# Performance work log

Measured on AMD Instinct MI355X. Metric: run time of the kernel, lower is better.

The kernel has to match this reference:

```python
import jax, jax.numpy as jnp
import numpy as np

N_EMBD = 768
N_HEAD = 12
B, T = 2, 2048
EPS = 1e-5


def _layernorm(x, g, b):
    mu = jnp.mean(x, axis=-1, keepdims=True)
    var = jnp.var(x, axis=-1, keepdims=True)
    return (x - mu) * jax.lax.rsqrt(var + EPS) * g + b


def _mha(q, k, v, causal):
    # q,k,v: [B,T,C] already projected
    Bq, Tq, C = q.shape
    d = C // N_HEAD
    q = q.reshape(Bq, Tq, N_HEAD, d).transpose(0, 2, 1, 3)  # b h t d
    k = k.reshape(Bq, Tq, N_HEAD, d).transpose(0, 2, 1, 3)
    v = v.reshape(Bq, Tq, N_HEAD, d).transpose(0, 2, 1, 3)
    scores = jnp.einsum('bhqd,bhkd->bhqk', q, k) * (1.0 / jnp.sqrt(jnp.float32(d)))
    if causal:
        mask = jnp.tril(jnp.ones((Tq, Tq), dtype=bool))
        scores = jnp.where(mask[None, None], scores, jnp.float32(-jnp.inf))
    att = jax.nn.softmax(scores, axis=-1)
    y = jnp.einsum('bhqk,bhkd->bhqd', att, v)
    return y.transpose(0, 2, 1, 3).reshape(Bq, Tq, C)


def setup_inputs() -> dict:
    key = jax.random.key(0)
    ks = iter(jax.random.split(key, 32))
    C = N_EMBD

    def lin(kk, din, dout):
        w = jax.random.normal(kk, (din, dout), jnp.float32) * (1.0 / np.sqrt(din))
        return w

    inp = {
        'x': jax.random.normal(next(ks), (B, T, C), jnp.float32),
        'encoder_output': jax.random.normal(next(ks), (B, T, C), jnp.float32),
        'ln1_g': jnp.ones((C,), jnp.float32), 'ln1_b': jnp.zeros((C,), jnp.float32),
        'attn_qkv_w': lin(next(ks), C, 3 * C), 'attn_qkv_b': jnp.zeros((3 * C,), jnp.float32),
        'attn_proj_w': lin(next(ks), C, C), 'attn_proj_b': jnp.zeros((C,), jnp.float32),
        'ln2_g': jnp.ones((C,), jnp.float32), 'ln2_b': jnp.zeros((C,), jnp.float32),
        'ca_q_w': lin(next(ks), C, C), 'ca_q_b': jnp.zeros((C,), jnp.float32),
        'ca_k_w': lin(next(ks), C, C), 'ca_k_b': jnp.zeros((C,), jnp.float32),
        'ca_v_w': lin(next(ks), C, C), 'ca_v_b': jnp.zeros((C,), jnp.float32),
        'ca_o_w': lin(next(ks), C, C), 'ca_o_b': jnp.zeros((C,), jnp.float32),
        'ln3_g': jnp.ones((C,), jnp.float32), 'ln3_b': jnp.zeros((C,), jnp.float32),
        'fc_w': lin(next(ks), C, 4 * C), 'fc_b': jnp.zeros((4 * C,), jnp.float32),
        'fc2_w': lin(next(ks), 4 * C, C), 'fc2_b': jnp.zeros((C,), jnp.float32),
    }
    return inp


def reference(x, encoder_output, ln1_g, ln1_b, attn_qkv_w, attn_qkv_b,
              attn_proj_w, attn_proj_b, ln2_g, ln2_b,
              ca_q_w, ca_q_b, ca_k_w, ca_k_b, ca_v_w, ca_v_b, ca_o_w, ca_o_b,
              ln3_g, ln3_b, fc_w, fc_b, fc2_w, fc2_b):
    C = N_EMBD
    # causal self-attention
    qkv = x @ attn_qkv_w + attn_qkv_b
    q, k, v = qkv[..., :C], qkv[..., C:2 * C], qkv[..., 2 * C:]
    sa = _mha(q, k, v, causal=True) @ attn_proj_w + attn_proj_b
    x = _layernorm(sa + x, ln1_g, ln1_b)
    # cross-attention
    cq = x @ ca_q_w + ca_q_b
    ck = encoder_output @ ca_k_w + ca_k_b
    cv = encoder_output @ ca_v_w + ca_v_b
    ca = _mha(cq, ck, cv, causal=False) @ ca_o_w + ca_o_b
    x = _layernorm(ca + x, ln2_g, ln2_b)
    # MLP
    h = jax.nn.relu(x @ fc_w + fc_b) @ fc2_w + fc2_b
    x = _layernorm(h + x, ln3_g, ln3_b)
    return x
```

## Files before the change

kernel.cpp:

```cpp
#include <hip/hip_runtime.h>


#define C_EMBD 768
#define NHEAD  12
#define HD     64
#define TB     2048
#define BB     2
#define MTOK   (BB*TB)

typedef __bf16 bf16_8 __attribute__((ext_vector_type(8)));
typedef float  f32x4  __attribute__((ext_vector_type(4)));

#define EXP2(x) exp2f(x)

__device__ __forceinline__ unsigned short f2bf(float f) {
    union { __bf16 h; unsigned short u; } c;
    c.h = (__bf16)f;
    return c.u;
}

#define GLOAD_LDS16(gsrc, ldst) \
    __builtin_amdgcn_global_load_lds( \
        (const __attribute__((address_space(1))) void*)(gsrc), \
        (__attribute__((address_space(3))) void*)(ldst), 16, 0, 0)

__global__ __launch_bounds__(256) void k_conv_bf16(const float* __restrict__ in,
                                                   unsigned short* __restrict__ out) {
    int i = blockIdx.x * 256 + threadIdx.x;
    float4 v = ((const float4*)in)[i];
    ushort4 o;
    o.x = f2bf(v.x); o.y = f2bf(v.y); o.z = f2bf(v.z); o.w = f2bf(v.w);
    ((ushort4*)out)[i] = o;
}

__global__ __launch_bounds__(256) void k_concat_bias(const float* __restrict__ a,
                                                     const float* __restrict__ b,
                                                     float* __restrict__ dst) {
    int i = blockIdx.x * 256 + threadIdx.x;
    if (i < C_EMBD) { dst[i] = a[i]; dst[C_EMBD + i] = b[i]; }
}

__global__ __launch_bounds__(256) void k_scale_bias(const float* __restrict__ b,
                                                    float* __restrict__ dst,
                                                    int n, float s, int lim) {
    int i = blockIdx.x * 256 + threadIdx.x;
    if (i < n) dst[i] = b[i] * (i < lim ? s : 1.0f);
}

__global__ __launch_bounds__(256) void k_transpose_w(const float* __restrict__ W,
                                                     unsigned short* __restrict__ Wt,
                                                     int K, int N,
                                                     float scale, int scaleLim) {
    __shared__ float tile[32][33];
    int tx = threadIdx.x, ty = threadIdx.y;
    int n0 = blockIdx.x * 32, k0 = blockIdx.y * 32;
#pragma unroll
    for (int i = 0; i < 4; ++i)
        tile[ty + 8*i][tx] = W[(size_t)(k0 + ty + 8*i) * N + n0 + tx];
    __syncthreads();
#pragma unroll
    for (int i = 0; i < 4; ++i) {
        int nrow = n0 + ty + 8*i;
        float s = (nrow < scaleLim) ? scale : 1.0f;
        Wt[(size_t)nrow * K + k0 + tx] = f2bf(tile[tx][ty + 8*i] * s);
    }
}

template<int BM, bool OUT_BF16, bool ADD_RES, bool RELU>
__global__ __launch_bounds__(256) void k_gemm_bt(
        const unsigned short* __restrict__ A,
        const unsigned short* __restrict__ Bt,
        const float* __restrict__ bias,
        const float* __restrict__ res,
        void* __restrict__ Cout,
        int M, int N, int K) {
    constexpr int MF = BM / 32;
    __shared__ unsigned short As[BM * 32];
    __shared__ unsigned short Bs[128 * 32];
    int tid  = threadIdx.x;
    int lane = tid & 63, wave = tid >> 6;
    int l16 = lane & 15, lg = lane >> 4;
    int wm = (wave >> 1) * (BM / 2), wn = (wave & 1) * 64;
    int bm = blockIdx.x * BM, bn = blockIdx.y * 128;

    f32x4 acc[MF][4] = {};

    for (int k0 = 0; k0 < K; k0 += 32) {
        __syncthreads();
#pragma unroll
        for (int i = 0; i < BM / 64; ++i) {
            int chunk = i * 256 + tid;
            GLOAD_LDS16(A + (size_t)(bm + (chunk >> 2)) * K + k0 + (chunk & 3) * 8,
                        As + (size_t)(i * 256 + wave * 64) * 8);
        }
#pragma unroll
        for (int i = 0; i < 2; ++i) {
            int chunk = i * 256 + tid;
            GLOAD_LDS16(Bt + (size_t)(bn + (chunk >> 2)) * K + k0 + (chunk & 3) * 8,
                        Bs + (size_t)(i * 256 + wave * 64) * 8);
        }
        __syncthreads();
        bf16_8 af[MF], bfr[4];
#pragma unroll
        for (int m = 0; m < MF; ++m)
            af[m]  = *(const bf16_8*)(As + (size_t)(wm + m*16 + l16) * 32 + lg * 8);
#pragma unroll
        for (int n = 0; n < 4; ++n)
            bfr[n] = *(const bf16_8*)(Bs + (size_t)(wn + n*16 + l16) * 32 + lg * 8);
#pragma unroll
        for (int m = 0; m < MF; ++m)
#pragma unroll
            for (int n = 0; n < 4; ++n)
                acc[m][n] = __builtin_amdgcn_mfma_f32_16x16x32_bf16(af[m], bfr[n], acc[m][n], 0, 0, 0);
    }

#pragma unroll
    for (int m = 0; m < MF; ++m) {
#pragma unroll
        for (int n = 0; n < 4; ++n) {
            int col = bn + wn + n*16 + l16;
            float bv = bias[col];
#pragma unroll
            for (int r = 0; r < 4; ++r) {
                int row = bm + wm + m*16 + lg*4 + r;
                float v = acc[m][n][r] + bv;
                if (ADD_RES) v += res[(size_t)row * N + col];
                if (RELU)    v = fmaxf(v, 0.f);
                if (OUT_BF16) ((unsigned short*)Cout)[(size_t)row * N + col] = f2bf(v);
                else          ((float*)Cout)[(size_t)row * N + col] = v;
            }
        }
    }
}

template<bool CAUSAL>
__global__ __launch_bounds__(256) void k_attn(
        const unsigned short* __restrict__ Qp,
        const unsigned short* __restrict__ Kp,
        const unsigned short* __restrict__ Vp,
        unsigned short* __restrict__ Yp,
        int strideQ, int strideKV) {
    __shared__ __bf16 Ks[64][72];
    __shared__ __bf16 Vt[64][72];
    __shared__ __bf16 Ps[4][16][72];
    int tid  = threadIdx.x;
    int lane = tid & 63, wave = tid >> 6;
    int l16 = lane & 15, lg = lane >> 4;
    int bh = blockIdx.y;
    int b = bh / NHEAD, h = bh - b * NHEAD;
    int qt = CAUSAL ? (gridDim.x - 1 - blockIdx.x) : blockIdx.x;
    int wq = qt * 64 + wave * 16;

    const unsigned short* Qb = Qp + (size_t)b * TB * strideQ  + h * HD;
    const unsigned short* Kb = Kp + (size_t)b * TB * strideKV + h * HD;
    const unsigned short* Vb = Vp + (size_t)b * TB * strideKV + h * HD;

    bf16_8 qf0 = *(const bf16_8*)(Qb + (size_t)(wq + l16) * strideQ + lg * 8);
    bf16_8 qf1 = *(const bf16_8*)(Qb + (size_t)(wq + l16) * strideQ + 32 + lg * 8);

    bf16_8 vones;
#pragma unroll
    for (int j = 0; j < 8; ++j) vones[j] = (__bf16)1.0f;

    int kr = tid >> 3, kc = (tid & 7) * 8;
    int vk2 = (tid & 31) * 2;
    int vd0 = (tid >> 5) * 8;

    const unsigned short* gK0 = Kb + (size_t)kr  * strideKV + kc;
    const unsigned short* gK1 = gK0 + (size_t)32 * strideKV;
    const unsigned short* gV0 = Vb + (size_t)vk2 * strideKV + vd0;
    const unsigned short* gV1 = gV0 + strideKV;
    const size_t stepKV = (size_t)64 * strideKV;

    int4 kA = *(const int4*)gK0;
    int4 kB = *(const int4*)gK1;
    unsigned vp[8];
    {
        int4 va = *(const int4*)gV0, vb2 = *(const int4*)gV1;
        const unsigned short* pa = (const unsigned short*)&va;
        const unsigned short* pb = (const unsigned short*)&vb2;
#pragma unroll
        for (int j = 0; j < 8; ++j) vp[j] = (unsigned)pa[j] | ((unsigned)pb[j] << 16);
    }

    f32x4 o[4] = {};
    float m_run[4], l_run[4];
#pragma unroll
    for (int r = 0; r < 4; ++r) { m_run[r] = -1e30f; l_run[r] = 0.f; }

    int ktEnd = CAUSAL ? (qt + 1) : (TB / 64);
    for (int kt = 0; kt < ktEnd; ++kt) {
        __syncthreads();
        *(int4*)(&Ks[kr][kc])      = kA;
        *(int4*)(&Ks[kr + 32][kc]) = kB;
#pragma unroll
        for (int j = 0; j < 8; ++j)
            *(unsigned*)(&Vt[vd0 + j][vk2]) = vp[j];
        __syncthreads();

        if (kt + 1 < ktEnd) {
            gK0 += stepKV; gK1 += stepKV; gV0 += stepKV; gV1 += stepKV;
            kA = *(const int4*)gK0;
            kB = *(const int4*)gK1;
            int4 va = *(const int4*)gV0, vb2 = *(const int4*)gV1;
            const unsigned short* pa = (const unsigned short*)&va;
            const unsigned short* pb = (const unsigned short*)&vb2;
#pragma unroll
            for (int j = 0; j < 8; ++j) vp[j] = (unsigned)pa[j] | ((unsigned)pb[j] << 16);
        }

        f32x4 s[4];
#pragma unroll
        for (int n = 0; n < 4; ++n) {
            f32x4 z = {};
            bf16_8 kf0 = *(const bf16_8*)(&Ks[n*16 + l16][lg*8]);
            bf16_8 kf1 = *(const bf16_8*)(&Ks[n*16 + l16][32 + lg*8]);
            z = __builtin_amdgcn_mfma_f32_16x16x32_bf16(qf0, kf0, z, 0, 0, 0);
            z = __builtin_amdgcn_mfma_f32_16x16x32_bf16(qf1, kf1, z, 0, 0, 0);
            s[n] = z;
        }
        if (CAUSAL && kt == qt) {
#pragma unroll
            for (int n = 0; n < 4; ++n)
#pragma unroll
                for (int r = 0; r < 4; ++r)
                    if (kt*64 + n*16 + l16 > wq + lg*4 + r) s[n][r] = -1e30f;
        }
        float mx[4];
#pragma unroll
        for (int r = 0; r < 4; ++r)
            mx[r] = fmaxf(fmaxf(s[0][r], s[1][r]), fmaxf(s[2][r], s[3][r]));
#pragma unroll
        for (int off = 1; off < 16; off <<= 1)
#pragma unroll
            for (int r = 0; r < 4; ++r)
                mx[r] = fmaxf(mx[r], __shfl_xor(mx[r], off, 64));
        bool big = (mx[0] > m_run[0] + 8.f) | (mx[1] > m_run[1] + 8.f) |
                   (mx[2] > m_run[2] + 8.f) | (mx[3] > m_run[3] + 8.f);
        if (__any(big)) {
#pragma unroll
            for (int r = 0; r < 4; ++r) {
                float mnew = fmaxf(m_run[r], mx[r]);
                float sf = EXP2(m_run[r] - mnew);
                m_run[r] = mnew;
                l_run[r] *= sf;
#pragma unroll
                for (int n = 0; n < 4; ++n) o[n][r] *= sf;
            }
        }
#pragma unroll
        for (int n = 0; n < 4; ++n)
#pragma unroll
            for (int r = 0; r < 4; ++r)
                Ps[wave][lg*4 + r][n*16 + l16] = (__bf16)EXP2(s[n][r] - m_run[r]);

        f32x4 zsum = {};
#pragma unroll
        for (int kk = 0; kk < 2; ++kk) {
            bf16_8 pa = *(const bf16_8*)(&Ps[wave][l16][kk*32 + lg*8]);
            zsum = __builtin_amdgcn_mfma_f32_16x16x32_bf16(pa, vones, zsum, 0, 0, 0);
#pragma unroll
            for (int n = 0; n < 4; ++n) {
                bf16_8 vf = *(const bf16_8*)(&Vt[n*16 + l16][kk*32 + lg*8]);
                o[n] = __builtin_amdgcn_mfma_f32_16x16x32_bf16(pa, vf, o[n], 0, 0, 0);
            }
        }
#pragma unroll
        for (int r = 0; r < 4; ++r) l_run[r] += zsum[r];
    }

#pragma unroll
    for (int r = 0; r < 4; ++r) {
        float rl = 1.0f / l_run[r];
        int token = b * TB + wq + lg*4 + r;
#pragma unroll
        for (int n = 0; n < 4; ++n)
            Yp[(size_t)token * C_EMBD + h * HD + n*16 + l16] = f2bf(o[n][r] * rl);
    }
}

template<bool WF32, bool WBF16>
__global__ __launch_bounds__(256) void k_ln(const float* __restrict__ in,
                                            const float* __restrict__ g,
                                            const float* __restrict__ bb,
                                            float* __restrict__ outf,
                                            unsigned short* __restrict__ outb) {
    int row = blockIdx.x;
    const float* x = in + (size_t)row * C_EMBD;
    float v[3], s1 = 0.f, s2 = 0.f;
#pragma unroll
    for (int i = 0; i < 3; ++i) {
        v[i] = x[threadIdx.x + i * 256];
        s1 += v[i];
        s2 += v[i] * v[i];
    }
#pragma unroll
    for (int off = 1; off < 64; off <<= 1) {
        s1 += __shfl_xor(s1, off, 64);
        s2 += __shfl_xor(s2, off, 64);
    }
    __shared__ float red[8];
    int wave = threadIdx.x >> 6, lane = threadIdx.x & 63;
    if (lane == 0) { red[wave] = s1; red[4 + wave] = s2; }
    __syncthreads();
    s1 = red[0] + red[1] + red[2] + red[3];
    s2 = red[4] + red[5] + red[6] + red[7];
    float mu  = s1 * (1.f / C_EMBD);
    float var = s2 * (1.f / C_EMBD) - mu * mu;
    float rs  = rsqrtf(var + 1e-5f);
#pragma unroll
    for (int i = 0; i < 3; ++i) {
        int c = threadIdx.x + i * 256;
        float y = (v[i] - mu) * rs * g[c] + bb[c];
        if (WF32)  outf[(size_t)row * C_EMBD + c] = y;
        if (WBF16) outb[(size_t)row * C_EMBD + c] = f2bf(y);
    }
}

extern "C" void kernel_launch(void* const* d_in, const int* in_sizes, int n_in,
                              void* d_out, int out_size, void* d_ws, size_t ws_size,
                              hipStream_t stream) {
    (void)in_sizes; (void)n_in; (void)out_size; (void)ws_size;
    const float* x      = (const float*)d_in[0];
    const float* enc    = (const float*)d_in[1];
    const float* ln1_g  = (const float*)d_in[2];
    const float* ln1_b  = (const float*)d_in[3];
    const float* qkv_w  = (const float*)d_in[4];
    const float* qkv_b  = (const float*)d_in[5];
    const float* proj_w = (const float*)d_in[6];
    const float* proj_b = (const float*)d_in[7];
    const float* ln2_g  = (const float*)d_in[8];
    const float* ln2_b  = (const float*)d_in[9];
    const float* caq_w  = (const float*)d_in[10];
    const float* caq_b  = (const float*)d_in[11];
    const float* cak_w  = (const float*)d_in[12];
    const float* cak_b  = (const float*)d_in[13];
    const float* cav_w  = (const float*)d_in[14];
    const float* cav_b  = (const float*)d_in[15];
    const float* cao_w  = (const float*)d_in[16];
    const float* cao_b  = (const float*)d_in[17];
    const float* ln3_g  = (const float*)d_in[18];
    const float* ln3_b  = (const float*)d_in[19];
    const float* fc_w   = (const float*)d_in[20];
    const float* fc_b   = (const float*)d_in[21];
    const float* fc2_w  = (const float*)d_in[22];
    const float* fc2_b  = (const float*)d_in[23];
    float* out = (float*)d_out;

    char* ws = (char*)d_ws;
    auto us = [&](size_t off) { return (unsigned short*)(ws + off); };
    auto fl = [&](size_t off) { return (float*)(ws + off); };

    const size_t O_WQKV  = 0;
    const size_t O_WPROJ = 3538944;
    const size_t O_WCQ   = 4718592;
    const size_t O_WCK   = 5898240;
    const size_t O_WCV   = 7077888;
    const size_t O_WCO   = 8257536;
    const size_t O_WFC   = 9437184;
    const size_t O_WFC2  = 14155776;
    const size_t O_XBF   = 18874368;
    const size_t O_ENCBF = 25165824;
    const size_t O_QKVBF = 31457280;
    const size_t O_Q2    = O_QKVBF;
    const size_t O_KV2   = O_QKVBF + 6291456;
    const size_t O_YBF   = 50331648;
    const size_t O_RESF  = 56623104;
    const size_t O_X1F   = 69206016;
    const size_t O_X1BF  = 81788928;
    const size_t O_X2F   = 88080384;
    const size_t O_X2BF  = 100663296;
    const size_t O_HBF   = 106954752;
    const size_t O_BKV   = O_HBF;
    const size_t O_BQKV  = O_HBF + 8192;
    const size_t O_BCQ   = O_HBF + 20480;

    const float SC2 = 0.125f * 1.44269504f;
    dim3 tb(32, 8);

    k_conv_bf16<<<3072, 256, 0, stream>>>(x,   us(O_XBF));
    k_conv_bf16<<<3072, 256, 0, stream>>>(enc, us(O_ENCBF));
    k_concat_bias<<<3, 256, 0, stream>>>(cak_b, cav_b, fl(O_BKV));
    k_scale_bias<<<9, 256, 0, stream>>>(qkv_b, fl(O_BQKV), 2304, SC2, 768);
    k_scale_bias<<<3, 256, 0, stream>>>(caq_b, fl(O_BCQ),   768, SC2, 768);

    k_transpose_w<<<dim3(2304/32,  768/32), tb, 0, stream>>>(qkv_w,  us(O_WQKV),  768, 2304, SC2, 768);
    k_transpose_w<<<dim3( 768/32,  768/32), tb, 0, stream>>>(proj_w, us(O_WPROJ), 768,  768, 1.f, 0);
    k_transpose_w<<<dim3( 768/32,  768/32), tb, 0, stream>>>(caq_w,  us(O_WCQ),   768,  768, SC2, 768);
    k_transpose_w<<<dim3( 768/32,  768/32), tb, 0, stream>>>(cak_w,  us(O_WCK),   768,  768, 1.f, 0);
    k_transpose_w<<<dim3( 768/32,  768/32), tb, 0, stream>>>(cav_w,  us(O_WCV),   768,  768, 1.f, 0);
    k_transpose_w<<<dim3( 768/32,  768/32), tb, 0, stream>>>(cao_w,  us(O_WCO),   768,  768, 1.f, 0);
    k_transpose_w<<<dim3(3072/32,  768/32), tb, 0, stream>>>(fc_w,   us(O_WFC),   768, 3072, 1.f, 0);
    k_transpose_w<<<dim3( 768/32, 3072/32), tb, 0, stream>>>(fc2_w,  us(O_WFC2), 3072,  768, 1.f, 0);

    k_gemm_bt<128, true,  false, false><<<dim3(32, 18), 256, 0, stream>>>(
        us(O_XBF), us(O_WQKV), fl(O_BQKV), nullptr, us(O_QKVBF), MTOK, 2304, 768);
    k_attn<true><<<dim3(TB/64, BB*NHEAD), 256, 0, stream>>>(
        us(O_QKVBF), us(O_QKVBF) + 768, us(O_QKVBF) + 1536, us(O_YBF), 2304, 2304);
    k_gemm_bt<64, false, true,  false><<<dim3(64, 6), 256, 0, stream>>>(
        us(O_YBF), us(O_WPROJ), proj_b, x, fl(O_RESF), MTOK, 768, 768);
    k_ln<true, true><<<MTOK, 256, 0, stream>>>(fl(O_RESF), ln1_g, ln1_b, fl(O_X1F), us(O_X1BF));
    k_gemm_bt<64, true,  false, false><<<dim3(64, 6), 256, 0, stream>>>(
        us(O_X1BF),  us(O_WCQ), fl(O_BCQ), nullptr, us(O_Q2), MTOK, 768, 768);
    k_gemm_bt<128, true,  false, false><<<dim3(32, 12), 256, 0, stream>>>(
        us(O_ENCBF), us(O_WCK), fl(O_BKV), nullptr, us(O_KV2), MTOK, 1536, 768);
    k_attn<false><<<dim3(TB/64, BB*NHEAD), 256, 0, stream>>>(
        us(O_Q2), us(O_KV2), us(O_KV2) + 768, us(O_YBF), 768, 1536);
    k_gemm_bt<64, false, true,  false><<<dim3(64, 6), 256, 0, stream>>>(
        us(O_YBF), us(O_WCO), cao_b, fl(O_X1F), fl(O_RESF), MTOK, 768, 768);
    k_ln<true, true><<<MTOK, 256, 0, stream>>>(fl(O_RESF), ln2_g, ln2_b, fl(O_X2F), us(O_X2BF));
    k_gemm_bt<128, true,  false, true ><<<dim3(32, 24), 256, 0, stream>>>(
        us(O_X2BF), us(O_WFC), fc_b, nullptr, us(O_HBF), MTOK, 3072, 768);
    k_gemm_bt<64, false, true,  false><<<dim3(64, 6), 256, 0, stream>>>(
        us(O_HBF), us(O_WFC2), fc2_b, fl(O_X2F), fl(O_RESF), MTOK, 768, 3072);
    k_ln<true, false><<<MTOK, 256, 0, stream>>>(fl(O_RESF), ln3_g, ln3_b, out, nullptr);
}
```

Baseline: 531.2 us.

## Fuse preprocessing launches and pair causal attention tiles per block

All weight transposes, input bf16 conversions and bias preparation are merged into one kernel that picks its job from the block index, replacing thirteen small launches with one. The causal attention grid is halved, and each block now handles query tile i and its mirror tile 31-i in sequence, so every block does about the same number of KV iterations. This is meant to cut launch overhead and the tail imbalance of triangular work. In exchange there are fewer blocks (384) to spread across the CUs, and the two passes run serially inside each block.

```diff
diff --git a/kernel.cpp b/kernel.cpp
--- a/kernel.cpp
+++ b/kernel.cpp
@@ -24,45 +24,67 @@
         (const __attribute__((address_space(1))) void*)(gsrc), \
         (__attribute__((address_space(3))) void*)(ldst), 16, 0, 0)
 
-__global__ __launch_bounds__(256) void k_conv_bf16(const float* __restrict__ in,
-                                                   unsigned short* __restrict__ out) {
-    int i = blockIdx.x * 256 + threadIdx.x;
-    float4 v = ((const float4*)in)[i];
-    ushort4 o;
-    o.x = f2bf(v.x); o.y = f2bf(v.y); o.z = f2bf(v.z); o.w = f2bf(v.w);
-    ((ushort4*)out)[i] = o;
-}
-
-__global__ __launch_bounds__(256) void k_concat_bias(const float* __restrict__ a,
-                                                     const float* __restrict__ b,
-                                                     float* __restrict__ dst) {
-    int i = blockIdx.x * 256 + threadIdx.x;
-    if (i < C_EMBD) { dst[i] = a[i]; dst[C_EMBD + i] = b[i]; }
-}
-
-__global__ __launch_bounds__(256) void k_scale_bias(const float* __restrict__ b,
-                                                    float* __restrict__ dst,
-                                                    int n, float s, int lim) {
-    int i = blockIdx.x * 256 + threadIdx.x;
-    if (i < n) dst[i] = b[i] * (i < lim ? s : 1.0f);
-}
-
-__global__ __launch_bounds__(256) void k_transpose_w(const float* __restrict__ W,
-                                                     unsigned short* __restrict__ Wt,
-                                                     int K, int N,
-                                                     float scale, int scaleLim) {
+__global__ __launch_bounds__(256) void k_preproc(
+        const float* __restrict__ x,     const float* __restrict__ enc,
+        const float* __restrict__ qkv_w, const float* __restrict__ proj_w,
+        const float* __restrict__ caq_w, const float* __restrict__ cak_w,
+        const float* __restrict__ cav_w, const float* __restrict__ cao_w,
+        const float* __restrict__ fc_w,  const float* __restrict__ fc2_w,
+        const float* __restrict__ qkv_b, const float* __restrict__ caq_b,
+        const float* __restrict__ cak_b, const float* __restrict__ cav_b,
+        unsigned short* __restrict__ xbf,  unsigned short* __restrict__ encbf,
+        unsigned short* __restrict__ wqkv, unsigned short* __restrict__ wproj,
+        unsigned short* __restrict__ wcq,  unsigned short* __restrict__ wck,
+        unsigned short* __restrict__ wcv,  unsigned short* __restrict__ wco,
+        unsigned short* __restrict__ wfc,  unsigned short* __restrict__ wfc2,
+        float* __restrict__ bqkv, float* __restrict__ bkv, float* __restrict__ bcq,
+        float sc2) {
     __shared__ float tile[32][33];
-    int tx = threadIdx.x, ty = threadIdx.y;
-    int n0 = blockIdx.x * 32, k0 = blockIdx.y * 32;
-#pragma unroll
-    for (int i = 0; i < 4; ++i)
-        tile[ty + 8*i][tx] = W[(size_t)(k0 + ty + 8*i) * N + n0 + tx];
-    __syncthreads();
-#pragma unroll
-    for (int i = 0; i < 4; ++i) {
-        int nrow = n0 + ty + 8*i;
-        float s = (nrow < scaleLim) ? scale : 1.0f;
-        Wt[(size_t)nrow * K + k0 + tx] = f2bf(tile[tx][ty + 8*i] * s);
+    int b = blockIdx.x, tid = threadIdx.x;
+    if (b < 9216) {
+        const float* W; unsigned short* Wt; int K, N, t; float sc; int slim;
+        if      (b < 1728) { W=qkv_w;  Wt=wqkv;  K=768;  N=2304; t=b;      sc=sc2; slim=768; }
+        else if (b < 2304) { W=proj_w; Wt=wproj; K=768;  N=768;  t=b-1728; sc=1.f; slim=0;   }
+        else if (b < 2880) { W=caq_w;  Wt=wcq;   K=768;  N=768;  t=b-2304; sc=sc2; slim=768; }
+        else if (b < 3456) { W=cak_w;  Wt=wck;   K=768;  N=768;  t=b-2880; sc=1.f; slim=0;   }
+        else if (b < 4032) { W=cav_w;  Wt=wcv;   K=768;  N=768;  t=b-3456; sc=1.f; slim=0;   }
+        else if (b < 4608) { W=cao_w;  Wt=wco;   K=768;  N=768;  t=b-4032; sc=1.f; slim=0;   }
+        else if (b < 6912) { W=fc_w;   Wt=wfc;   K=768;  N=3072; t=b-4608; sc=1.f; slim=0;   }
+        else               { W=fc2_w;  Wt=wfc2;  K=3072; N=768;  t=b-6912; sc=1.f; slim=0;   }
+        int ntx = N >> 5;
+        int n0 = (t % ntx) * 32, k0 = (t / ntx) * 32;
+        int tx = tid & 31, ty = tid >> 5;
+#pragma unroll
+        for (int i = 0; i < 4; ++i)
+            tile[ty + 8*i][tx] = W[(size_t)(k0 + ty + 8*i) * N + n0 + tx];
+        __syncthreads();
+#pragma unroll
+        for (int i = 0; i < 4; ++i) {
+            int nrow = n0 + ty + 8*i;
+            float s = (nrow < slim) ? sc : 1.0f;
+            Wt[(size_t)nrow * K + k0 + tx] = f2bf(tile[tx][ty + 8*i] * s);
+        }
+    } else if (b < 15360) {
+        int b2 = b - 9216;
+        const float* src = (b2 < 3072) ? x   : enc;
+        unsigned short* dst = (b2 < 3072) ? xbf : encbf;
+        int i = (b2 < 3072 ? b2 : b2 - 3072) * 256 + tid;
+        float4 v = ((const float4*)src)[i];
+        ushort4 o;
+        o.x = f2bf(v.x); o.y = f2bf(v.y); o.z = f2bf(v.z); o.w = f2bf(v.w);
+        ((ushort4*)dst)[i] = o;
+    } else {
+        int b3 = b - 15360;
+        if (b3 < 9) {
+            int i = b3 * 256 + tid;
+            if (i < 2304) bqkv[i] = qkv_b[i] * (i < 768 ? sc2 : 1.0f);
+        } else if (b3 < 12) {
+            int i = (b3 - 9) * 256 + tid;
+            if (i < 768) { bkv[i] = cak_b[i]; bkv[768 + i] = cav_b[i]; }
+        } else {
+            int i = (b3 - 12) * 256 + tid;
+            if (i < 768) bcq[i] = caq_b[i] * sc2;
+        }
     }
 }
 
@@ -148,16 +170,11 @@
     int l16 = lane & 15, lg = lane >> 4;
     int bh = blockIdx.y;
     int b = bh / NHEAD, h = bh - b * NHEAD;
-    int qt = CAUSAL ? (gridDim.x - 1 - blockIdx.x) : blockIdx.x;
-    int wq = qt * 64 + wave * 16;
 
     const unsigned short* Qb = Qp + (size_t)b * TB * strideQ  + h * HD;
     const unsigned short* Kb = Kp + (size_t)b * TB * strideKV + h * HD;
     const unsigned short* Vb = Vp + (size_t)b * TB * strideKV + h * HD;
 
-    bf16_8 qf0 = *(const bf16_8*)(Qb + (size_t)(wq + l16) * strideQ + lg * 8);
-    bf16_8 qf1 = *(const bf16_8*)(Qb + (size_t)(wq + l16) * strideQ + 32 + lg * 8);
-
     bf16_8 vones;
 #pragma unroll
     for (int j = 0; j < 8; ++j) vones[j] = (__bf16)1.0f;
@@ -165,43 +182,26 @@
     int kr = tid >> 3, kc = (tid & 7) * 8;
     int vk2 = (tid & 31) * 2;
     int vd0 = (tid >> 5) * 8;
-
-    const unsigned short* gK0 = Kb + (size_t)kr  * strideKV + kc;
-    const unsigned short* gK1 = gK0 + (size_t)32 * strideKV;
-    const unsigned short* gV0 = Vb + (size_t)vk2 * strideKV + vd0;
-    const unsigned short* gV1 = gV0 + strideKV;
     const size_t stepKV = (size_t)64 * strideKV;
 
-    int4 kA = *(const int4*)gK0;
-    int4 kB = *(const int4*)gK1;
-    unsigned vp[8];
-    {
-        int4 va = *(const int4*)gV0, vb2 = *(const int4*)gV1;
-        const unsigned short* pa = (const unsigned short*)&va;
-        const unsigned short* pb = (const unsigned short*)&vb2;
-#pragma unroll
-        for (int j = 0; j < 8; ++j) vp[j] = (unsigned)pa[j] | ((unsigned)pb[j] << 16);
-    }
-
-    f32x4 o[4] = {};
-    float m_run[4], l_run[4];
-#pragma unroll
-    for (int r = 0; r < 4; ++r) { m_run[r] = -1e30f; l_run[r] = 0.f; }
-
-    int ktEnd = CAUSAL ? (qt + 1) : (TB / 64);
-    for (int kt = 0; kt < ktEnd; ++kt) {
-        __syncthreads();
-        *(int4*)(&Ks[kr][kc])      = kA;
-        *(int4*)(&Ks[kr + 32][kc]) = kB;
-#pragma unroll
-        for (int j = 0; j < 8; ++j)
-            *(unsigned*)(&Vt[vd0 + j][vk2]) = vp[j];
-        __syncthreads();
-
-        if (kt + 1 < ktEnd) {
-            gK0 += stepKV; gK1 += stepKV; gV0 += stepKV; gV1 += stepKV;
-            kA = *(const int4*)gK0;
-            kB = *(const int4*)gK1;
+    const int npass = CAUSAL ? 2 : 1;
+    for (int pass = 0; pass < npass; ++pass) {
+        int qt = CAUSAL ? (pass == 0 ? (TB/64 - 1 - (int)blockIdx.x) : (int)blockIdx.x)
+                        : (int)blockIdx.x;
+        int wq = qt * 64 + wave * 16;
+
+        bf16_8 qf0 = *(const bf16_8*)(Qb + (size_t)(wq + l16) * strideQ + lg * 8);
+        bf16_8 qf1 = *(const bf16_8*)(Qb + (size_t)(wq + l16) * strideQ + 32 + lg * 8);
+
+        const unsigned short* gK0 = Kb + (size_t)kr  * strideKV + kc;
+        const unsigned short* gK1 = gK0 + (size_t)32 * strideKV;
+        const unsigned short* gV0 = Vb + (size_t)vk2 * strideKV + vd0;
+        const unsigned short* gV1 = gV0 + strideKV;
+
+        int4 kA = *(const int4*)gK0;
+        int4 kB = *(const int4*)gK1;
+        unsigned vp[8];
+        {
             int4 va = *(const int4*)gV0, vb2 = *(const int4*)gV1;
             const unsigned short* pa = (const unsigned short*)&va;
             const unsigned short* pb = (const unsigned short*)&vb2;
@@ -209,73 +209,100 @@
             for (int j = 0; j < 8; ++j) vp[j] = (unsigned)pa[j] | ((unsigned)pb[j] << 16);
         }
 
-        f32x4 s[4];
-#pragma unroll
-        for (int n = 0; n < 4; ++n) {
-            f32x4 z = {};
-            bf16_8 kf0 = *(const bf16_8*)(&Ks[n*16 + l16][lg*8]);
-            bf16_8 kf1 = *(const bf16_8*)(&Ks[n*16 + l16][32 + lg*8]);
-            z = __builtin_amdgcn_mfma_f32_16x16x32_bf16(qf0, kf0, z, 0, 0, 0);
-            z = __builtin_amdgcn_mfma_f32_16x16x32_bf16(qf1, kf1, z, 0, 0, 0);
-            s[n] = z;
-        }
-        if (CAUSAL && kt == qt) {
+        f32x4 o[4] = {};
+        float m_run[4], l_run[4];
+#pragma unroll
+        for (int r = 0; r < 4; ++r) { m_run[r] = -1e30f; l_run[r] = 0.f; }
+
+        int ktEnd = CAUSAL ? (qt + 1) : (TB / 64);
+        for (int kt = 0; kt < ktEnd; ++kt) {
+            __syncthreads();
+            *(int4*)(&Ks[kr][kc])      = kA;
+            *(int4*)(&Ks[kr + 32][kc]) = kB;
+#pragma unroll
+            for (int j = 0; j < 8; ++j)
+                *(unsigned*)(&Vt[vd0 + j][vk2]) = vp[j];
+            __syncthreads();
+
+            if (kt + 1 < ktEnd) {
+                gK0 += stepKV; gK1 += stepKV; gV0 += stepKV; gV1 += stepKV;
+                kA = *(const int4*)gK0;
+                kB = *(const int4*)gK1;
+                int4 va = *(const int4*)gV0, vb2 = *(const int4*)gV1;
+                const unsigned short* pa = (const unsigned short*)&va;
+                const unsigned short* pb = (const unsigned short*)&vb2;
+#pragma unroll
+                for (int j = 0; j < 8; ++j) vp[j] = (unsigned)pa[j] | ((unsigned)pb[j] << 16);
+            }
+
+            f32x4 s[4];
+#pragma unroll
+            for (int n = 0; n < 4; ++n) {
+                f32x4 z = {};
+                bf16_8 kf0 = *(const bf16_8*)(&Ks[n*16 + l16][lg*8]);
+                bf16_8 kf1 = *(const bf16_8*)(&Ks[n*16 + l16][32 + lg*8]);
+                z = __builtin_amdgcn_mfma_f32_16x16x32_bf16(qf0, kf0, z, 0, 0, 0);
+                z = __builtin_amdgcn_mfma_f32_16x16x32_bf16(qf1, kf1, z, 0, 0, 0);
+                s[n] = z;
+            }
+            if (CAUSAL && kt == qt) {
+#pragma unroll
+                for (int n = 0; n < 4; ++n)
+#pragma unroll
+                    for (int r = 0; r < 4; ++r)
+                        if (kt*64 + n*16 + l16 > wq + lg*4 + r) s[n][r] = -1e30f;
+            }
+            float mx[4];
+#pragma unroll
+            for (int r = 0; r < 4; ++r)
+                mx[r] = fmaxf(fmaxf(s[0][r], s[1][r]), fmaxf(s[2][r], s[3][r]));
+#pragma unroll
+            for (int off = 1; off < 16; off <<= 1)
+#pragma unroll
+                for (int r = 0; r < 4; ++r)
+                    mx[r] = fmaxf(mx[r], __shfl_xor(mx[r], off, 64));
+            bool big = (mx[0] > m_run[0] + 8.f) | (mx[1] > m_run[1] + 8.f) |
+                       (mx[2] > m_run[2] + 8.f) | (mx[3] > m_run[3] + 8.f);
+            if (__any(big)) {
+#pragma unroll
+                for (int r = 0; r < 4; ++r) {
+                    float mnew = fmaxf(m_run[r], mx[r]);
+                    float sf = EXP2(m_run[r] - mnew);
+                    m_run[r] = mnew;
+                    l_run[r] *= sf;
+#pragma unroll
+                    for (int n = 0; n < 4; ++n) o[n][r] *= sf;
+                }
+            }
 #pragma unroll
             for (int n = 0; n < 4; ++n)
 #pragma unroll
                 for (int r = 0; r < 4; ++r)
-                    if (kt*64 + n*16 + l16 > wq + lg*4 + r) s[n][r] = -1e30f;
-        }
-        float mx[4];
-#pragma unroll
-        for (int r = 0; r < 4; ++r)
-            mx[r] = fmaxf(fmaxf(s[0][r], s[1][r]), fmaxf(s[2][r], s[3][r]));
-#pragma unroll
-        for (int off = 1; off < 16; off <<= 1)
-#pragma unroll
-            for (int r = 0; r < 4; ++r)
-                mx[r] = fmaxf(mx[r], __shfl_xor(mx[r], off, 64));
-        bool big = (mx[0] > m_run[0] + 8.f) | (mx[1] > m_run[1] + 8.f) |
-                   (mx[2] > m_run[2] + 8.f) | (mx[3] > m_run[3] + 8.f);
-        if (__any(big)) {
-#pragma unroll
-            for (int r = 0; r < 4; ++r) {
-                float mnew = fmaxf(m_run[r], mx[r]);
-                float sf = EXP2(m_run[r] - mnew);
-                m_run[r] = mnew;
-                l_run[r] *= sf;
-#pragma unroll
-                for (int n = 0; n < 4; ++n) o[n][r] *= sf;
-            }
-        }
-#pragma unroll
-        for (int n = 0; n < 4; ++n)
-#pragma unroll
-            for (int r = 0; r < 4; ++r)
-                Ps[wave][lg*4 + r][n*16 + l16] = (__bf16)EXP2(s[n][r] - m_run[r]);
-
-        f32x4 zsum = {};
-#pragma unroll
-        for (int kk = 0; kk < 2; ++kk) {
-            bf16_8 pa = *(const bf16_8*)(&Ps[wave][l16][kk*32 + lg*8]);
-            zsum = __builtin_amdgcn_mfma_f32_16x16x32_bf16(pa, vones, zsum, 0, 0, 0);
-#pragma unroll
-            for (int n = 0; n < 4; ++n) {
-                bf16_8 vf = *(const bf16_8*)(&Vt[n*16 + l16][kk*32 + lg*8]);
-                o[n] = __builtin_amdgcn_mfma_f32_16x16x32_bf16(pa, vf, o[n], 0, 0, 0);
-            }
-        }
-#pragma unroll
-        for (int r = 0; r < 4; ++r) l_run[r] += zsum[r];
-    }
-
-#pragma unroll
-    for (int r = 0; r < 4; ++r) {
-        float rl = 1.0f / l_run[r];
-        int token = b * TB + wq + lg*4 + r;
-#pragma unroll
-        for (int n = 0; n < 4; ++n)
-            Yp[(size_t)token * C_EMBD + h * HD + n*16 + l16] = f2bf(o[n][r] * rl);
+                    Ps[wave][lg*4 + r][n*16 + l16] = (__bf16)EXP2(s[n][r] - m_run[r]);
+
+            f32x4 zsum = {};
+#pragma unroll
+            for (int kk = 0; kk < 2; ++kk) {
+                bf16_8 pa = *(const bf16_8*)(&Ps[wave][l16][kk*32 + lg*8]);
+                zsum = __builtin_amdgcn_mfma_f32_16x16x32_bf16(pa, vones, zsum, 0, 0, 0);
+#pragma unroll
+                for (int n = 0; n < 4; ++n) {
+                    bf16_8 vf = *(const bf16_8*)(&Vt[n*16 + l16][kk*32 + lg*8]);
+                    o[n] = __builtin_amdgcn_mfma_f32_16x16x32_bf16(pa, vf, o[n], 0, 0, 0);
+                }
+            }
+#pragma unroll
+            for (int r = 0; r < 4; ++r) l_run[r] += zsum[r];
+        }
+
+#pragma unroll
+        for (int r = 0; r < 4; ++r) {
+            float rl = 1.0f / l_run[r];
+            int token = b * TB + wq + lg*4 + r;
+#pragma unroll
+            for (int n = 0; n < 4; ++n)
+                Yp[(size_t)token * C_EMBD + h * HD + n*16 + l16] = f2bf(o[n][r] * rl);
+        }
     }
 }
 
@@ -376,26 +403,18 @@
     const size_t O_BCQ   = O_HBF + 20480;
 
     const float SC2 = 0.125f * 1.44269504f;
-    dim3 tb(32, 8);
-
-    k_conv_bf16<<<3072, 256, 0, stream>>>(x,   us(O_XBF));
-    k_conv_bf16<<<3072, 256, 0, stream>>>(enc, us(O_ENCBF));
-    k_concat_bias<<<3, 256, 0, stream>>>(cak_b, cav_b, fl(O_BKV));
-    k_scale_bias<<<9, 256, 0, stream>>>(qkv_b, fl(O_BQKV), 2304, SC2, 768);
-    k_scale_bias<<<3, 256, 0, stream>>>(caq_b, fl(O_BCQ),   768, SC2, 768);
-
-    k_transpose_w<<<dim3(2304/32,  768/32), tb, 0, stream>>>(qkv_w,  us(O_WQKV),  768, 2304, SC2, 768);
-    k_transpose_w<<<dim3( 768/32,  768/32), tb, 0, stream>>>(proj_w, us(O_WPROJ), 768,  768, 1.f, 0);
-    k_transpose_w<<<dim3( 768/32,  768/32), tb, 0, stream>>>(caq_w,  us(O_WCQ),   768,  768, SC2, 768);
-    k_transpose_w<<<dim3( 768/32,  768/32), tb, 0, stream>>>(cak_w,  us(O_WCK),   768,  768, 1.f, 0);
-    k_transpose_w<<<dim3( 768/32,  768/32), tb, 0, stream>>>(cav_w,  us(O_WCV),   768,  768, 1.f, 0);
-    k_transpose_w<<<dim3( 768/32,  768/32), tb, 0, stream>>>(cao_w,  us(O_WCO),   768,  768, 1.f, 0);
-    k_transpose_w<<<dim3(3072/32,  768/32), tb, 0, stream>>>(fc_w,   us(O_WFC),   768, 3072, 1.f, 0);
-    k_transpose_w<<<dim3( 768/32, 3072/32), tb, 0, stream>>>(fc2_w,  us(O_WFC2), 3072,  768, 1.f, 0);
+
+    k_preproc<<<15375, 256, 0, stream>>>(
+        x, enc, qkv_w, proj_w, caq_w, cak_w, cav_w, cao_w, fc_w, fc2_w,
+        qkv_b, caq_b, cak_b, cav_b,
+        us(O_XBF), us(O_ENCBF),
+        us(O_WQKV), us(O_WPROJ), us(O_WCQ), us(O_WCK),
+        us(O_WCV), us(O_WCO), us(O_WFC), us(O_WFC2),
+        fl(O_BQKV), fl(O_BKV), fl(O_BCQ), SC2);
 
     k_gemm_bt<128, true,  false, false><<<dim3(32, 18), 256, 0, stream>>>(
         us(O_XBF), us(O_WQKV), fl(O_BQKV), nullptr, us(O_QKVBF), MTOK, 2304, 768);
-    k_attn<true><<<dim3(TB/64, BB*NHEAD), 256, 0, stream>>>(
+    k_attn<true><<<dim3(TB/128, BB*NHEAD), 256, 0, stream>>>(
         us(O_QKVBF), us(O_QKVBF) + 768, us(O_QKVBF) + 1536, us(O_YBF), 2304, 2304);
     k_gemm_bt<64, false, true,  false><<<dim3(64, 6), 256, 0, stream>>>(
         us(O_YBF), us(O_WPROJ), proj_b, x, fl(O_RESF), MTOK, 768, 768);
```

New measurement: 496.8 us. -6.5%, faster.
